# Kernel optimization log

Hardware: AMD Instinct MI355X
Metric: run time of the kernel (lower is better)

Reference implementation:

```python
import jax, jax.numpy as jnp
import numpy as np

D_MODEL = 1024
EXPAND = 2
HEADDIM = 64
D_STATE = 128
D_CONV = 4
D_INNER = EXPAND * D_MODEL          # 2048
NHEADS = D_INNER // HEADDIM         # 32
CONV_DIM = D_INNER + 2 * D_STATE    # x, B, C share the depthwise conv
EPS = 1e-5


def setup_inputs() -> dict:
    key = jax.random.key(0)
    ks = jax.random.split(key, 8)
    d_in_proj = 2 * D_INNER + 2 * D_STATE + NHEADS
    x = jax.random.normal(ks[0], (2, 2048, D_MODEL), jnp.float32)
    W_in = jax.random.normal(ks[1], (D_MODEL, d_in_proj), jnp.float32) * (D_MODEL ** -0.5)
    conv_w = jax.random.normal(ks[2], (CONV_DIM, D_CONV), jnp.float32) * 0.2
    conv_b = jnp.zeros((CONV_DIM,), jnp.float32)
    # dt init: softplus(dt_bias) in [1e-3, 1e-1]  (inverse-softplus init, as in mamba_ssm)
    dt = jnp.exp(jax.random.uniform(ks[3], (NHEADS,), jnp.float32,
                                    minval=np.log(1e-3), maxval=np.log(1e-1)))
    dt_bias = dt + jnp.log(-jnp.expm1(-dt))
    A_log = jnp.log(jax.random.uniform(ks[4], (NHEADS,), jnp.float32, minval=1.0, maxval=16.0))
    D = jnp.ones((NHEADS,), jnp.float32)
    norm_w = jnp.ones((D_INNER,), jnp.float32)
    W_out = jax.random.normal(ks[5], (D_INNER, D_MODEL), jnp.float32) * (D_INNER ** -0.5)
    return dict(x=x, W_in=W_in, conv_w=conv_w, conv_b=conv_b, dt_bias=dt_bias,
                A_log=A_log, D=D, norm_w=norm_w, W_out=W_out)


def _causal_depthwise_conv(u, w, b):
    # u: (B, L, C), w: (C, K) depthwise, causal (pad K-1 on the left)
    B, L, C = u.shape
    up = jnp.pad(u, ((0, 0), (D_CONV - 1, 0), (0, 0)))
    y = b
    for k in range(D_CONV):
        y = y + up[:, k:k + L, :] * w[:, k]
    return y


def _rms(v):
    return v * jax.lax.rsqrt(jnp.mean(v * v, axis=-1, keepdims=True) + EPS)


def reference(x, W_in, conv_w, conv_b, dt_bias, A_log, D, norm_w, W_out):
    b, l, _ = x.shape
    zxbcdt = x @ W_in                                  # (b, l, 2*d_inner + 2*d_state + nheads)
    z = zxbcdt[..., :D_INNER]
    xBC = zxbcdt[..., D_INNER:D_INNER + CONV_DIM]
    dt = jax.nn.softplus(zxbcdt[..., -NHEADS:] + dt_bias)   # (b, l, h)
    xBC = jax.nn.silu(_causal_depthwise_conv(xBC, conv_w, conv_b))
    xs = xBC[..., :D_INNER].reshape(b, l, NHEADS, HEADDIM)  # (b, l, h, p)
    Bm = xBC[..., D_INNER:D_INNER + D_STATE]                 # (b, l, n)
    Cm = xBC[..., D_INNER + D_STATE:]                        # (b, l, n)
    A = -jnp.exp(A_log)                                      # (h,)
    decay = jnp.exp(dt * A)                                  # (b, l, h)

    def step(h, inp):
        dec_t, dt_t, x_t, B_t, C_t = inp   # (b,h) (b,h) (b,h,p) (b,n) (b,n)
        h = h * dec_t[:, :, None, None] + (dt_t[:, :, None] * x_t)[..., None] * B_t[:, None, None, :]
        y_t = jnp.einsum('bhpn,bn->bhp', h, C_t)
        return h, y_t

    h0 = jnp.zeros((b, NHEADS, HEADDIM, D_STATE), x.dtype)
    xs_t = (decay.transpose(1, 0, 2), dt.transpose(1, 0, 2),
            xs.transpose(1, 0, 2, 3), Bm.transpose(1, 0, 2), Cm.transpose(1, 0, 2))
    _, ys = jax.lax.scan(step, h0, xs_t)                     # ys: (l, b, h, p)
    y = ys.transpose(1, 0, 2, 3) + D[None, None, :, None] * xs
    y = y.reshape(b, l, D_INNER)
    # gated RMSNorm (RMSNormGated in mamba_ssm), then out projection
    y = _rms(y * jax.nn.silu(z)) * norm_w
    out = y @ W_out                                          # (b, l, d_model)
    # wrapper: post RMSNorm (weight freshly initialized to ones) + residual
    return _rms(out) + x
```

## Files before the change

kernel.cpp:

```cpp
#include <hip/hip_runtime.h>
#include <hip/hip_bf16.h>

#define DMODEL 1024
#define DI     2048
#define DSTATE 128
#define NH     32
#define HD     64
#define CONVD  2304
#define LSEQ   2048
#define BATCH  2
#define DPROJ  4384
#define NPAD   4480
#define EPSV   1e-5f
#define QCH    128
#define NCH    16

#define AS1 __attribute__((address_space(1)))
#define AS3 __attribute__((address_space(3)))

typedef __attribute__((ext_vector_type(8))) short bf16x8;
typedef __attribute__((ext_vector_type(4))) float f32x4;

union U4 { ushort4 u; __hip_bfloat16 h[4]; };

__device__ __forceinline__ float bf2f(unsigned short u) {
  union { unsigned int i; float f; } c; c.i = ((unsigned)u) << 16; return c.f;
}
__device__ __forceinline__ ushort4 pack4(float x0, float x1, float x2, float x3) {
  U4 p;
  p.h[0] = __float2bfloat16(x0); p.h[1] = __float2bfloat16(x1);
  p.h[2] = __float2bfloat16(x2); p.h[3] = __float2bfloat16(x3);
  return p.u;
}

__device__ __forceinline__ bf16x8 ldsfrag(const __hip_bfloat16* base, int row, int ke) {
  int byte = row * 256 + ke * 2;
  byte ^= (row & 7) << 4;
  return *reinterpret_cast<const bf16x8*>(reinterpret_cast<const char*>(base) + byte);
}
__device__ __forceinline__ void ldswr4(__hip_bfloat16* base, int row, int col4, ushort4 v) {
  int byte = row * 256 + col4 * 2;
  byte ^= (row & 7) << 4;
  *reinterpret_cast<ushort4*>(reinterpret_cast<char*>(base) + byte) = v;
}
__device__ __forceinline__ void ldswr8(__hip_bfloat16* base, int row, int colElem,
                                       unsigned lo, unsigned hi) {
  int byte = row * 256 + colElem * 2;
  byte ^= (row & 7) << 4;
  uint2 v; v.x = lo; v.y = hi;
  *reinterpret_cast<uint2*>(reinterpret_cast<char*>(base) + byte) = v;
}
__device__ __forceinline__ bf16x8 frag32(const __hip_bfloat16* base, int row, int g) {
  int byte = row * 64 + (((g ^ (row >> 1)) & 3) << 4);
  return *reinterpret_cast<const bf16x8*>(reinterpret_cast<const char*>(base) + byte);
}

__device__ __forceinline__ void quadtr(unsigned a01, unsigned a23, int ql,
                                       unsigned& w01, unsigned& w23) {
  unsigned y01 = __shfl_xor((int)a01, 1), y23 = __shfl_xor((int)a23, 1);
  unsigned c01 = (ql & 1) ? ((y01 >> 16) | (a01 & 0xFFFF0000u))
                          : ((a01 & 0xFFFFu) | (y01 << 16));
  unsigned c23 = (ql & 1) ? ((y23 >> 16) | (a23 & 0xFFFF0000u))
                          : ((a23 & 0xFFFFu) | (y23 << 16));
  unsigned d01 = __shfl_xor((int)c01, 2), d23 = __shfl_xor((int)c23, 2);
  w01 = (ql & 2) ? d23 : c01;
  w23 = (ql & 2) ? c23 : d01;
}


__global__ void f32_to_bf16_kernel(const float* __restrict__ in,
                                   __hip_bfloat16* __restrict__ out, int n4) {
  int i = blockIdx.x * 256 + threadIdx.x;
  if (i >= n4) return;
  float4 v = reinterpret_cast<const float4*>(in)[i];
  reinterpret_cast<ushort4*>(out)[i] = pack4(v.x, v.y, v.z, v.w);
}

__global__ void transpose_f32_bf16(const float* __restrict__ in,
                                   __hip_bfloat16* __restrict__ out,
                                   int R, int C, int Cpad) {
  __shared__ float tile[32][33];
  int n0 = blockIdx.x * 32, k0 = blockIdx.y * 32;
  int tx = threadIdx.x, ty = threadIdx.y;
#pragma unroll
  for (int j = 0; j < 32; j += 8) {
    int k = k0 + ty + j, n = n0 + tx;
    tile[ty + j][tx] = (n < C) ? in[(size_t)k * C + n] : 0.f;
  }
  __syncthreads();
#pragma unroll
  for (int j = 0; j < 32; j += 8) {
    int n = n0 + ty + j, k = k0 + tx;
    if (n < Cpad) out[(size_t)n * R + k] = __float2bfloat16(tile[tx][ty + j]);
  }
}


template <int MODE>
__global__ __launch_bounds__(512, 2)
void gemm256_bt(const __hip_bfloat16* __restrict__ A,
                const __hip_bfloat16* __restrict__ Bt,
                __hip_bfloat16* __restrict__ Cout, int K) {
  __shared__ __hip_bfloat16 smA[4][256 * 32];
  __shared__ __hip_bfloat16 smB[4][256 * 32];
  int bm, bn, kbase, Kp;
  if constexpr (MODE == 0) {
    const int xcd = blockIdx.x & 7;
    const int i = blockIdx.x >> 3;
    bm = (xcd * 2 + (i & 1)) * 256;
    bn = (i >> 1) * 256;
    kbase = 0; Kp = K;
  } else {
    const int s = blockIdx.x >> 6;
    const int bb = blockIdx.x & 63;
    const int xcd = bb & 7;
    const int i = bb >> 3;
    bm = (xcd * 2 + (i & 1)) * 256;
    bn = (i >> 1) * 256;
    Kp = K >> 2; kbase = s * Kp;
  }
  const int tid = threadIdx.x;
  const int w = tid >> 6, lane = tid & 63;
  const int wm = w >> 2, wn = w & 3;
  const int fr = lane & 15, g = lane >> 4;
  const int srow = tid >> 2;
  const int sc = (((tid & 3) ^ ((srow >> 1) & 3)) << 3);

  f32x4 acc[8][4];
#pragma unroll
  for (int m = 0; m < 8; ++m)
#pragma unroll
    for (int n = 0; n < 4; ++n) acc[m][n] = (f32x4){0.f, 0.f, 0.f, 0.f};

  const __hip_bfloat16* aS = A + (size_t)(bm + srow) * K + kbase + sc;
  const __hip_bfloat16* bS = Bt + (size_t)(bn + srow) * K + kbase + sc;
  const int dbase = w * 512;

  auto STAGE = [&](int buf, int kt) {
    const int k0 = kt << 5;
#pragma unroll
    for (int j = 0; j < 2; ++j) {
      __builtin_amdgcn_global_load_lds((const AS1 void*)(aS + (size_t)(j * 128) * K + k0),
                                       (AS3 void*)(&smA[buf][j * 4096 + dbase]), 16, 0, 0);
      __builtin_amdgcn_global_load_lds((const AS1 void*)(bS + (size_t)(j * 128) * K + k0),
                                       (AS3 void*)(&smB[buf][j * 4096 + dbase]), 16, 0, 0);
    }
  };

  const int nt = Kp >> 5;
  STAGE(0, 0);
  STAGE(1, 1);
  for (int kt = 0; kt < nt; ++kt) {
    const int cur = kt & 3;
    if (kt + 2 < nt) {
      STAGE((kt + 2) & 3, kt + 2);
      asm volatile("s_waitcnt vmcnt(8)" ::: "memory");
    } else if (kt + 1 < nt) {
      asm volatile("s_waitcnt vmcnt(4)" ::: "memory");
    } else {
      asm volatile("s_waitcnt vmcnt(0)" ::: "memory");
    }
    __builtin_amdgcn_s_barrier();
    __builtin_amdgcn_s_setprio(1);
    bf16x8 af[8], bfv[4];
#pragma unroll
    for (int m = 0; m < 8; ++m)
      af[m] = frag32(&smA[cur][0], wm * 128 + m * 16 + fr, g);
#pragma unroll
    for (int n = 0; n < 4; ++n)
      bfv[n] = frag32(&smB[cur][0], wn * 64 + n * 16 + fr, g);
#pragma unroll
    for (int m = 0; m < 8; ++m)
#pragma unroll
      for (int n = 0; n < 4; ++n)
        acc[m][n] = __builtin_amdgcn_mfma_f32_16x16x32_bf16(af[m], bfv[n], acc[m][n], 0, 0, 0);
    __builtin_amdgcn_s_setprio(0);
  }

  const int rb = g * 4;
#pragma unroll
  for (int m = 0; m < 8; ++m)
#pragma unroll
    for (int n = 0; n < 4; ++n) {
      int row = bm + wm * 128 + m * 16 + rb;
      int col = bn + wn * 64 + n * 16 + fr;
      if constexpr (MODE == 0) {
        __hip_bfloat16* cp = Cout + (size_t)row * NPAD + col;
#pragma unroll
        for (int j = 0; j < 4; ++j)
          cp[(size_t)j * NPAD] = __float2bfloat16(acc[m][n][j]);
      } else {
        __hip_bfloat16* cp = Cout + (size_t)(blockIdx.x >> 6) * 4194304 +
                             (size_t)row * DMODEL + col;
#pragma unroll
        for (int j = 0; j < 4; ++j)
          cp[(size_t)j * DMODEL] = __float2bfloat16(acc[m][n][j]);
      }
    }
}


__global__ __launch_bounds__(256, 4)
void gemm_bt3(const __hip_bfloat16* __restrict__ A,
              const __hip_bfloat16* __restrict__ Bt,
              __hip_bfloat16* __restrict__ Cout, float* __restrict__ dtraw,
              int N, int K, int bnOff, int NT) {
  __shared__ __hip_bfloat16 smA[2][128 * 32];
  __shared__ __hip_bfloat16 smB[2][128 * 32];
  int bb = blockIdx.x;
  const int bm = (bb / NT) * 128;
  const int bn = bnOff + (bb % NT) * 128;
  const int t = threadIdx.x;
  const int w = t >> 6, lane = t & 63;
  const int wr = (w >> 1) * 64, wc = (w & 1) * 64;
  const int fr = lane & 15, g = lane >> 4;
  const int srow = lane >> 2;
  const int scol = ((lane & 3) ^ ((lane >> 3) & 3)) * 8;

  f32x4 acc[4][4];
#pragma unroll
  for (int m = 0; m < 4; ++m)
#pragma unroll
    for (int n = 0; n < 4; ++n) acc[m][n] = (f32x4){0.f, 0.f, 0.f, 0.f};

  const __hip_bfloat16* aSrc = A + (size_t)(bm + srow) * K + scol;
  const __hip_bfloat16* bSrc = Bt + (size_t)(bn + srow) * K + scol;

  auto STAGE = [&](int buf, int k0) {
#pragma unroll
    for (int j = 0; j < 2; ++j) {
      int ro = w * 32 + j * 16;
      __builtin_amdgcn_global_load_lds((const AS1 void*)(aSrc + (size_t)ro * K + k0),
                                       (AS3 void*)(&smA[buf][ro * 32]), 16, 0, 0);
      __builtin_amdgcn_global_load_lds((const AS1 void*)(bSrc + (size_t)ro * K + k0),
                                       (AS3 void*)(&smB[buf][ro * 32]), 16, 0, 0);
    }
  };

  STAGE(0, 0);
  __syncthreads();
  const int nt = K >> 5;
  int cur = 0;
  for (int kt = 0; kt < nt; ++kt) {
    if (kt + 1 < nt) STAGE(cur ^ 1, (kt + 1) << 5);
    bf16x8 af[4], bfv[4];
#pragma unroll
    for (int m = 0; m < 4; ++m) af[m] = frag32(&smA[cur][0], wr + m * 16 + fr, g);
#pragma unroll
    for (int n = 0; n < 4; ++n) bfv[n] = frag32(&smB[cur][0], wc + n * 16 + fr, g);
#pragma unroll
    for (int m = 0; m < 4; ++m)
#pragma unroll
      for (int n = 0; n < 4; ++n)
        acc[m][n] = __builtin_amdgcn_mfma_f32_16x16x32_bf16(af[m], bfv[n], acc[m][n], 0, 0, 0);
    __syncthreads();
    cur ^= 1;
  }

  const int r4 = g * 4;
  const int cn = lane & 15;
#pragma unroll
  for (int m = 0; m < 4; ++m)
#pragma unroll
    for (int n = 0; n < 4; ++n) {
      int row = bm + wr + m * 16 + r4;
      int col = bn + wc + n * 16 + cn;
      __hip_bfloat16* cp = Cout + (size_t)row * N + col;
#pragma unroll
      for (int j = 0; j < 4; ++j) {
        float v = acc[m][n][j];
        cp[(size_t)j * N] = __float2bfloat16(v);
        if (col >= DI + CONVD && col < DPROJ)
          dtraw[(size_t)(row + j) * NH + (col - (DI + CONVD))] = v;
      }
    }
}


__global__ __launch_bounds__(256)
void chunk_stats_kernel(const float* __restrict__ dtraw, const float* __restrict__ dt_bias,
                        const float* __restrict__ A_log,
                        float* __restrict__ csb, float* __restrict__ dtc,
                        float* __restrict__ swb, float* __restrict__ cumdecb,
                        float* __restrict__ pbuf) {
  int w = threadIdx.x >> 6, lane = threadIdx.x & 63;
  int bid = blockIdx.x * 4 + w;
  int c = bid & (NCH - 1);
  int h = (bid >> 4) & 31;
  int b = bid >> 9;
  int t0 = c * QCH;
  float a = expf(A_log[h]);
  float bias = dt_bias[h];
  const float* dtp = dtraw + ((size_t)b * LSEQ + t0) * NH + h;
  float r0 = dtp[lane * NH] + bias;
  float r1 = dtp[(64 + lane) * NH] + bias;
  float v0 = (r0 > 20.f) ? r0 : log1pf(expf(r0));
  float v1 = (r1 > 20.f) ? r1 : log1pf(expf(r1));
  float s0 = v0;
#pragma unroll
  for (int off = 1; off < 64; off <<= 1) {
    float tv = __shfl_up(s0, off);
    if (lane >= off) s0 += tv;
  }
  float T0 = __shfl(s0, 63);
  float s1 = v1;
#pragma unroll
  for (int off = 1; off < 64; off <<= 1) {
    float tv = __shfl_up(s1, off);
    if (lane >= off) s1 += tv;
  }
  float cs1 = s1 + T0;
  float Tt = __shfl(s1, 63) + T0;
  size_t base = (size_t)bid * 128;
  csb[base + lane] = s0;        csb[base + 64 + lane] = cs1;
  dtc[base + lane] = v0;        dtc[base + 64 + lane] = v1;
  swb[base + lane] = v0 * expf(-a * (Tt - s0));
  swb[base + 64 + lane] = v1 * expf(-a * (Tt - cs1));
  cumdecb[base + lane] = expf(-a * s0);
  cumdecb[base + 64 + lane] = expf(-a * cs1);
  if (lane == 0) pbuf[bid] = expf(-a * Tt);
}


__global__ __launch_bounds__(256)
void conv_silu_kernel(const __hip_bfloat16* __restrict__ zxb,
                      const float* __restrict__ cw,
                      const float* __restrict__ cb,
                      __hip_bfloat16* __restrict__ xbc) {
  int idx = blockIdx.x * 256 + threadIdx.x;
  if (idx >= BATCH * (LSEQ / 4) * (CONVD / 8)) return;
  int c8 = idx % (CONVD / 8);
  int bl4 = idx / (CONVD / 8);
  int l0 = (bl4 % (LSEQ / 4)) * 4;
  int b = bl4 / (LSEQ / 4);
  int c0 = c8 * 8;
  const __hip_bfloat16* src = zxb + (size_t)b * LSEQ * NPAD + DI + c0;

  float wv[8][4];
#pragma unroll
  for (int j = 0; j < 8; ++j)
    *reinterpret_cast<float4*>(wv[j]) = *reinterpret_cast<const float4*>(cw + (c0 + j) * 4);
  float bias[8];
  *reinterpret_cast<float4*>(bias) = *reinterpret_cast<const float4*>(cb + c0);
  *reinterpret_cast<float4*>(bias + 4) = *reinterpret_cast<const float4*>(cb + c0 + 4);

  float hist[7][8];
#pragma unroll
  for (int r = 0; r < 7; ++r) {
    int row = l0 - 3 + r;
    if (row >= 0) {
      uint4 v = *reinterpret_cast<const uint4*>(src + (size_t)row * NPAD);
      unsigned uu[4] = {v.x, v.y, v.z, v.w};
#pragma unroll
      for (int j = 0; j < 8; ++j)
        hist[r][j] = bf2f((j & 1) ? (unsigned short)(uu[j >> 1] >> 16)
                                  : (unsigned short)(uu[j >> 1] & 0xFFFF));
    } else {
#pragma unroll
      for (int j = 0; j < 8; ++j) hist[r][j] = 0.f;
    }
  }

#pragma unroll
  for (int t = 0; t < 4; ++t) {
    float acc[8];
#pragma unroll
    for (int j = 0; j < 8; ++j) {
      float a = bias[j];
      a = fmaf(wv[j][0], hist[t + 0][j], a);
      a = fmaf(wv[j][1], hist[t + 1][j], a);
      a = fmaf(wv[j][2], hist[t + 2][j], a);
      a = fmaf(wv[j][3], hist[t + 3][j], a);
      acc[j] = a / (1.f + expf(-a));
    }
    ushort4* dst = reinterpret_cast<ushort4*>(
        xbc + ((size_t)b * LSEQ + l0 + t) * CONVD + c0);
    dst[0] = pack4(acc[0], acc[1], acc[2], acc[3]);
    dst[1] = pack4(acc[4], acc[5], acc[6], acc[7]);
  }
}


__global__ __launch_bounds__(256, 2)
void ssd_mfma_local(const __hip_bfloat16* __restrict__ bxc,
                    const float* __restrict__ csb, const float* __restrict__ dtc,
                    const float* __restrict__ swb,
                    const float* __restrict__ A_log, const float* __restrict__ Dparm,
                    __hip_bfloat16* __restrict__ y, __hip_bfloat16* __restrict__ sbuf) {
  __shared__ __hip_bfloat16 T_B[128 * 128];
  __shared__ __hip_bfloat16 T_C[128 * 128];
  __shared__ __hip_bfloat16 T_X[64 * 128];

  const int bid = blockIdx.x;
  const int c = bid & (NCH - 1);
  const int h = (bid >> 4) & 31;
  const int b = bid >> 9;
  const int tid = threadIdx.x;
  const int w = tid >> 6, lane = tid & 63;
  const int q = lane >> 2, ql = lane & 3;
  const int t0 = c * QCH;
  const __hip_bfloat16* xc = bxc + (size_t)b * LSEQ * CONVD;
  const float a = expf(A_log[h]);
  const float Dh = Dparm[h];

  {
    const int rsub = lane >> 4;
    const int ch = lane & 15;
#pragma unroll
    for (int j = 0; j < 8; ++j) {
      int row = w * 32 + j * 4 + rsub;
      int sc_ = ch ^ (row & 7);
      const __hip_bfloat16* pB = xc + (size_t)(t0 + row) * CONVD + DI + sc_ * 8;
      __builtin_amdgcn_global_load_lds((const AS1 void*)pB,
                                       (AS3 void*)(T_B + (w * 32 + j * 4) * 128), 16, 0, 0);
      __builtin_amdgcn_global_load_lds((const AS1 void*)(pB + DSTATE),
                                       (AS3 void*)(T_C + (w * 32 + j * 4) * 128), 16, 0, 0);
    }
  }
#pragma unroll
  for (int r = 0; r < 8; ++r) {
    int gidx = w * 128 + q * 8 + r;
    int tb = (gidx & 31) * 4;
    int pb = (gidx >> 5) * 4;
    int t = tb + ql;
    ushort4 xv = *reinterpret_cast<const ushort4*>(xc + (size_t)(t0 + t) * CONVD + h * HD + pb);
    unsigned a01 = (unsigned)xv.x | ((unsigned)xv.y << 16);
    unsigned a23 = (unsigned)xv.z | ((unsigned)xv.w << 16);
    unsigned w01, w23;
    quadtr(a01, a23, ql, w01, w23);
    ldswr8(T_X, pb + ql, tb, w01, w23);
  }
  __syncthreads();

  const int fr = lane & 15;
  const int fk = (lane >> 4) * 8;
  const int rb = (lane >> 4) * 4;

  const int sR0 = (w >> 1) * 64, tC0 = (w & 1) * 64;
  f32x4 g[4][4];
#pragma unroll
  for (int m = 0; m < 4; ++m)
#pragma unroll
    for (int n = 0; n < 4; ++n) g[m][n] = (f32x4){0.f, 0.f, 0.f, 0.f};
  for (int kk = 0; kk < 128; kk += 32) {
    bf16x8 af[4], bfv[4];
#pragma unroll
    for (int m = 0; m < 4; ++m) af[m] = ldsfrag(T_B, sR0 + m * 16 + fr, kk + fk);
#pragma unroll
    for (int n = 0; n < 4; ++n) bfv[n] = ldsfrag(T_C, tC0 + n * 16 + fr, kk + fk);
#pragma unroll
    for (int m = 0; m < 4; ++m)
#pragma unroll
      for (int n = 0; n < 4; ++n)
        g[m][n] = __builtin_amdgcn_mfma_f32_16x16x32_bf16(af[m], bfv[n], g[m][n], 0, 0, 0);
  }
  __syncthreads();

  {
    const float* csp = csb + (size_t)bid * 128;
    const float* dtp = dtc + (size_t)bid * 128;
#pragma unroll
    for (int m = 0; m < 4; ++m) {
      int sb0 = sR0 + m * 16 + rb;
      float cs_s[4], dt_s[4];
#pragma unroll
      for (int j = 0; j < 4; ++j) { cs_s[j] = csp[sb0 + j]; dt_s[j] = dtp[sb0 + j]; }
#pragma unroll
      for (int n = 0; n < 4; ++n) {
        int tt = tC0 + n * 16 + fr;
        float cst = csp[tt];
        float vv[4];
#pragma unroll
        for (int j = 0; j < 4; ++j) {
          int s = sb0 + j;
          float e = __expf(-a * (cst - cs_s[j])) * dt_s[j];
          float pv = (s <= tt) ? g[m][n][j] * e : 0.f;
          vv[j] = pv + ((s == tt) ? Dh : 0.f);
        }
        ldswr4(T_B, tt, sb0, pack4(vv[0], vv[1], vv[2], vv[3]));
      }
    }
    const float* swp = swb + (size_t)bid * 128;
#pragma unroll
    for (int r = 0; r < 16; ++r) {
      int gidx = w * 256 + q * 16 + r;
      int tb = (gidx & 31) * 4;
      int nb = (gidx >> 5) * 4;
      int t = tb + ql;
      ushort4 bv = *reinterpret_cast<const ushort4*>(xc + (size_t)(t0 + t) * CONVD + DI + nb);
      float wt = swp[t];
      ushort4 sv = pack4(bf2f(bv.x) * wt, bf2f(bv.y) * wt, bf2f(bv.z) * wt, bf2f(bv.w) * wt);
      unsigned a01 = (unsigned)sv.x | ((unsigned)sv.y << 16);
      unsigned a23 = (unsigned)sv.z | ((unsigned)sv.w << 16);
      unsigned w01, w23;
      quadtr(a01, a23, ql, w01, w23);
      ldswr8(T_C, nb + ql, tb, w01, w23);
    }
  }
  __syncthreads();

  {
    int tR0 = w * 32;
    f32x4 yac[2][4];
#pragma unroll
    for (int m = 0; m < 2; ++m)
#pragma unroll
      for (int n = 0; n < 4; ++n) yac[m][n] = (f32x4){0.f, 0.f, 0.f, 0.f};
    for (int kk = 0; kk < 128; kk += 32) {
      bf16x8 af[2], bfv[4];
#pragma unroll
      for (int m = 0; m < 2; ++m) af[m] = ldsfrag(T_B, tR0 + m * 16 + fr, kk + fk);
#pragma unroll
      for (int n = 0; n < 4; ++n) bfv[n] = ldsfrag(T_X, n * 16 + fr, kk + fk);
#pragma unroll
      for (int m = 0; m < 2; ++m)
#pragma unroll
        for (int n = 0; n < 4; ++n)
          yac[m][n] = __builtin_amdgcn_mfma_f32_16x16x32_bf16(af[m], bfv[n], yac[m][n], 0, 0, 0);
    }
#pragma unroll
    for (int m = 0; m < 2; ++m)
#pragma unroll
      for (int n = 0; n < 4; ++n) {
        int trow = tR0 + m * 16 + rb;
        int pc = n * 16 + fr;
        __hip_bfloat16* yp = y + ((size_t)b * LSEQ + t0 + trow) * DI + h * HD + pc;
#pragma unroll
        for (int j = 0; j < 4; ++j)
          yp[(size_t)j * DI] = __float2bfloat16(yac[m][n][j]);
      }
  }

  {
    int pR0 = (w >> 1) * 32, nC0 = (w & 1) * 64;
    f32x4 sac[2][4];
#pragma unroll
    for (int m = 0; m < 2; ++m)
#pragma unroll
      for (int n = 0; n < 4; ++n) sac[m][n] = (f32x4){0.f, 0.f, 0.f, 0.f};
    for (int kk = 0; kk < 128; kk += 32) {
      bf16x8 af[2], bfv[4];
#pragma unroll
      for (int m = 0; m < 2; ++m) af[m] = ldsfrag(T_X, pR0 + m * 16 + fr, kk + fk);
#pragma unroll
      for (int n = 0; n < 4; ++n) bfv[n] = ldsfrag(T_C, nC0 + n * 16 + fr, kk + fk);
#pragma unroll
      for (int m = 0; m < 2; ++m)
#pragma unroll
        for (int n = 0; n < 4; ++n)
          sac[m][n] = __builtin_amdgcn_mfma_f32_16x16x32_bf16(af[m], bfv[n], sac[m][n], 0, 0, 0);
    }
    __hip_bfloat16* sg = sbuf + (size_t)bid * 8192;
#pragma unroll
    for (int m = 0; m < 2; ++m)
#pragma unroll
      for (int n = 0; n < 4; ++n) {
        int p = pR0 + m * 16 + rb;
        int nn = nC0 + n * 16 + fr;
#pragma unroll
        for (int j = 0; j < 4; ++j)
          sg[(size_t)(p + j) * 128 + nn] = __float2bfloat16(sac[m][n][j]);
      }
  }
}


__global__ void ssd_prop_kernel(__hip_bfloat16* __restrict__ sbuf,
                                const float* __restrict__ pbuf) {
  int idx = blockIdx.x * 256 + threadIdx.x;
  int bh = idx >> 13;
  int e = idx & 8191;
  __hip_bfloat16* base = sbuf + (size_t)bh * NCH * 8192 + e;
  const float* pb = pbuf + bh * NCH;
  float hs = 0.f;
  for (int cc = 0; cc < NCH; ++cc) {
    float sc = __bfloat162float(base[(size_t)cc * 8192]);
    base[(size_t)cc * 8192] = __float2bfloat16(hs);
    hs = fmaf(hs, pb[cc], sc);
  }
}


__global__ __launch_bounds__(256, 4)
void ssd_mfma_corr(const __hip_bfloat16* __restrict__ bxc, const __hip_bfloat16* __restrict__ sbuf,
                   const float* __restrict__ cumdecb, __hip_bfloat16* __restrict__ y) {
  const int bid = (blockIdx.x / 15) * 16 + 1 + (blockIdx.x % 15);
  const int h = (bid >> 4) & 31;
  const int b = bid >> 9;
  const int tid = threadIdx.x;
  const int w = tid >> 6, lane = tid & 63;
  const int t0 = (bid & (NCH - 1)) * QCH;
  const __hip_bfloat16* xc = bxc + (size_t)b * LSEQ * CONVD;
  const __hip_bfloat16* hsb = sbuf + (size_t)bid * 8192;
  const int fr = lane & 15;
  const int fk = (lane >> 4) * 8;
  const int rb = (lane >> 4) * 4;
  const int tR0 = w * 32;

  f32x4 ac[2][4];
#pragma unroll
  for (int m = 0; m < 2; ++m)
#pragma unroll
    for (int n = 0; n < 4; ++n) ac[m][n] = (f32x4){0.f, 0.f, 0.f, 0.f};

#pragma unroll
  for (int kk = 0; kk < 128; kk += 32) {
    bf16x8 af[2], bfv[4];
#pragma unroll
    for (int m = 0; m < 2; ++m)
      af[m] = *reinterpret_cast<const bf16x8*>(
          xc + (size_t)(t0 + tR0 + m * 16 + fr) * CONVD + DI + DSTATE + kk + fk);
#pragma unroll
    for (int n = 0; n < 4; ++n)
      bfv[n] = *reinterpret_cast<const bf16x8*>(hsb + (size_t)(n * 16 + fr) * 128 + kk + fk);
#pragma unroll
    for (int m = 0; m < 2; ++m)
#pragma unroll
      for (int n = 0; n < 4; ++n)
        ac[m][n] = __builtin_amdgcn_mfma_f32_16x16x32_bf16(af[m], bfv[n], ac[m][n], 0, 0, 0);
  }

  const float* cdp = cumdecb + (size_t)bid * 128;
#pragma unroll
  for (int m = 0; m < 2; ++m) {
    int trow = tR0 + m * 16 + rb;
    float cd[4];
#pragma unroll
    for (int j = 0; j < 4; ++j) cd[j] = cdp[trow + j];
#pragma unroll
    for (int n = 0; n < 4; ++n) {
      int pc = n * 16 + fr;
      __hip_bfloat16* yp = y + ((size_t)b * LSEQ + t0 + trow) * DI + h * HD + pc;
#pragma unroll
      for (int j = 0; j < 4; ++j) {
        float old = __bfloat162float(yp[(size_t)j * DI]);
        yp[(size_t)j * DI] = __float2bfloat16(old + cd[j] * ac[m][n][j]);
      }
    }
  }
}


__global__ __launch_bounds__(256)
void gate_rms_kernel(const __hip_bfloat16* __restrict__ y, const __hip_bfloat16* __restrict__ zxb,
                     const float* __restrict__ nw, __hip_bfloat16* __restrict__ g) {
  int row = blockIdx.x;
  int t = threadIdx.x;
  int c0 = t * 8;
  const __hip_bfloat16* yr = y + (size_t)row * DI + c0;
  const __hip_bfloat16* zr = zxb + (size_t)row * NPAD + c0;
  ushort4 y0 = *reinterpret_cast<const ushort4*>(yr);
  ushort4 y1 = *reinterpret_cast<const ushort4*>(yr + 4);
  ushort4 z0 = *reinterpret_cast<const ushort4*>(zr);
  ushort4 z1 = *reinterpret_cast<const ushort4*>(zr + 4);
  float zf[8] = {bf2f(z0.x), bf2f(z0.y), bf2f(z0.z), bf2f(z0.w),
                 bf2f(z1.x), bf2f(z1.y), bf2f(z1.z), bf2f(z1.w)};
  float yf[8] = {bf2f(y0.x), bf2f(y0.y), bf2f(y0.z), bf2f(y0.w),
                 bf2f(y1.x), bf2f(y1.y), bf2f(y1.z), bf2f(y1.w)};
  float v[8];
  float ss = 0.f;
#pragma unroll
  for (int j = 0; j < 8; ++j) {
    float z = zf[j];
    float vv = yf[j] * (z / (1.f + expf(-z)));
    v[j] = vv;
    ss += vv * vv;
  }
#pragma unroll
  for (int off = 32; off; off >>= 1) ss += __shfl_down(ss, off);
  __shared__ float red[4];
  if ((t & 63) == 0) red[t >> 6] = ss;
  __syncthreads();
  float tot = red[0] + red[1] + red[2] + red[3];
  float rstd = rsqrtf(tot * (1.f / DI) + EPSV);
  float4 na = *reinterpret_cast<const float4*>(nw + c0);
  float4 nb = *reinterpret_cast<const float4*>(nw + c0 + 4);
  ushort4 o0 = pack4(v[0] * rstd * na.x, v[1] * rstd * na.y,
                     v[2] * rstd * na.z, v[3] * rstd * na.w);
  ushort4 o1v = pack4(v[4] * rstd * nb.x, v[5] * rstd * nb.y,
                      v[6] * rstd * nb.z, v[7] * rstd * nb.w);
  ushort4* gp = reinterpret_cast<ushort4*>(g + (size_t)row * DI + c0);
  gp[0] = o0;
  gp[1] = o1v;
}


__global__ __launch_bounds__(256)
void final_rms_add(const __hip_bfloat16* __restrict__ o1p, const float* __restrict__ x,
                   float* __restrict__ out) {
  int row = blockIdx.x;
  int t = threadIdx.x;
  int c0 = t * 4;
  size_t off = (size_t)row * DMODEL + c0;
  float4 o = {0.f, 0.f, 0.f, 0.f};
#pragma unroll
  for (int s = 0; s < 4; ++s) {
    ushort4 p = *reinterpret_cast<const ushort4*>(o1p + (size_t)s * 4194304 + off);
    o.x += bf2f(p.x); o.y += bf2f(p.y); o.z += bf2f(p.z); o.w += bf2f(p.w);
  }
  float ss = o.x * o.x + o.y * o.y + o.z * o.z + o.w * o.w;
#pragma unroll
  for (int off2 = 32; off2; off2 >>= 1) ss += __shfl_down(ss, off2);
  __shared__ float red[4];
  if ((t & 63) == 0) red[t >> 6] = ss;
  __syncthreads();
  float tot = red[0] + red[1] + red[2] + red[3];
  float rstd = rsqrtf(tot * (1.f / DMODEL) + EPSV);
  float4 xv = *reinterpret_cast<const float4*>(x + off);
  float4 r;
  r.x = o.x * rstd + xv.x;
  r.y = o.y * rstd + xv.y;
  r.z = o.z * rstd + xv.z;
  r.w = o.w * rstd + xv.w;
  *reinterpret_cast<float4*>(out + off) = r;
}


extern "C" void kernel_launch(void* const* d_in, const int* in_sizes, int n_in,
                              void* d_out, int out_size, void* d_ws, size_t ws_size,
                              hipStream_t stream) {
  const float* x       = (const float*)d_in[0];
  const float* W_in    = (const float*)d_in[1];
  const float* conv_w  = (const float*)d_in[2];
  const float* conv_b  = (const float*)d_in[3];
  const float* dt_bias = (const float*)d_in[4];
  const float* A_log   = (const float*)d_in[5];
  const float* Dp      = (const float*)d_in[6];
  const float* norm_w  = (const float*)d_in[7];
  const float* W_out   = (const float*)d_in[8];
  float* out = (float*)d_out;

  float* zxF  = (float*)d_ws;
  __hip_bfloat16* zxb = (__hip_bfloat16*)zxF;
  __hip_bfloat16* o1p = zxb;
  float* xbcF = zxF + (size_t)18350080;
  __hip_bfloat16* xbc = (__hip_bfloat16*)xbcF;
  float* ybufF = xbcF + (size_t)9437184;
  __hip_bfloat16* ybuf = (__hip_bfloat16*)ybufF;
  float* dtraw = ybufF + (size_t)8388608;
  float* cumdecb = dtraw + (size_t)131072;
  __hip_bfloat16* xbf   = (__hip_bfloat16*)(cumdecb + 131072);
  __hip_bfloat16* wtin  = xbf + (size_t)4194304;
  __hip_bfloat16* wtout = wtin + (size_t)4587520;
  float* pbuf = (float*)(wtout + (size_t)2097152);
  float* csb  = pbuf + 1024;
  float* dtc  = csb + (size_t)131072;
  float* swb  = dtc + (size_t)131072;
  __hip_bfloat16* sbuf = xbf;
  __hip_bfloat16* gbf = xbf;

  f32_to_bf16_kernel<<<4096, 256, 0, stream>>>(x, xbf, 1048576);
  transpose_f32_bf16<<<dim3(140, 32), dim3(32, 8), 0, stream>>>(W_in, wtin, 1024, 4384, 4480);
  transpose_f32_bf16<<<dim3(32, 64), dim3(32, 8), 0, stream>>>(W_out, wtout, 2048, 1024, 1024);

  gemm256_bt<0><<<256, 512, 0, stream>>>(xbf, wtin, zxb, 1024);
  gemm_bt3<<<96, 256, 0, stream>>>(xbf, wtin, zxb, dtraw, NPAD, 1024, 4096, 3);

  chunk_stats_kernel<<<256, 256, 0, stream>>>(dtraw, dt_bias, A_log, csb, dtc, swb, cumdecb, pbuf);
  conv_silu_kernel<<<1152, 256, 0, stream>>>(zxb, conv_w, conv_b, xbc);

  ssd_mfma_local<<<1024, 256, 0, stream>>>(xbc, csb, dtc, swb, A_log, Dp, ybuf, sbuf);
  ssd_prop_kernel<<<2048, 256, 0, stream>>>(sbuf, pbuf);
  ssd_mfma_corr<<<960, 256, 0, stream>>>(xbc, sbuf, cumdecb, ybuf);

  gate_rms_kernel<<<4096, 256, 0, stream>>>(ybuf, zxb, norm_w, gbf);

  gemm256_bt<1><<<256, 512, 0, stream>>>(gbf, wtout, o1p, 2048);

  final_rms_add<<<4096, 256, 0, stream>>>(o1p, x, out);
}
```

Baseline: 201.8 us.

## Merge input prep kernels into one launch and retile conv to 4ch x 8 steps

Combines the x-to-bf16 cast and both weight transposes into a single prep kernel dispatched by block index, removing two kernel launches and their gaps. Separately, the causal conv kernel now handles 4 channels over 8 time steps per thread instead of 8 channels over 4 steps. This cuts redundant halo row reads per output but uses narrower 8-byte loads and stores. The prep merge adds a branch per block.

```diff
diff --git a/kernel.cpp b/kernel.cpp
--- a/kernel.cpp
+++ b/kernel.cpp
@@ -68,20 +68,31 @@
 }
 
 
-__global__ void f32_to_bf16_kernel(const float* __restrict__ in,
-                                   __hip_bfloat16* __restrict__ out, int n4) {
-  int i = blockIdx.x * 256 + threadIdx.x;
-  if (i >= n4) return;
-  float4 v = reinterpret_cast<const float4*>(in)[i];
-  reinterpret_cast<ushort4*>(out)[i] = pack4(v.x, v.y, v.z, v.w);
-}
-
-__global__ void transpose_f32_bf16(const float* __restrict__ in,
-                                   __hip_bfloat16* __restrict__ out,
-                                   int R, int C, int Cpad) {
+__global__ __launch_bounds__(256)
+void prep_kernel(const float* __restrict__ x, __hip_bfloat16* __restrict__ xbf,
+                 const float* __restrict__ W_in, __hip_bfloat16* __restrict__ wtin,
+                 const float* __restrict__ W_out, __hip_bfloat16* __restrict__ wtout) {
   __shared__ float tile[32][33];
-  int n0 = blockIdx.x * 32, k0 = blockIdx.y * 32;
-  int tx = threadIdx.x, ty = threadIdx.y;
+  const int b = blockIdx.x, tid = threadIdx.x;
+  if (b < 4096) {
+    int i = b * 256 + tid;
+    float4 v = reinterpret_cast<const float4*>(x)[i];
+    reinterpret_cast<ushort4*>(xbf)[i] = pack4(v.x, v.y, v.z, v.w);
+    return;
+  }
+  const float* in;
+  __hip_bfloat16* outp;
+  int R, C, Cpad, n0, k0;
+  if (b < 4096 + 4480) {
+    int t = b - 4096;
+    in = W_in; outp = wtin; R = 1024; C = 4384; Cpad = 4480;
+    n0 = (t % 140) * 32; k0 = (t / 140) * 32;
+  } else {
+    int t = b - 8576;
+    in = W_out; outp = wtout; R = 2048; C = 1024; Cpad = 1024;
+    n0 = (t % 32) * 32; k0 = (t / 32) * 32;
+  }
+  int tx = tid & 31, ty = tid >> 5;
 #pragma unroll
   for (int j = 0; j < 32; j += 8) {
     int k = k0 + ty + j, n = n0 + tx;
@@ -91,7 +102,7 @@
 #pragma unroll
   for (int j = 0; j < 32; j += 8) {
     int n = n0 + ty + j, k = k0 + tx;
-    if (n < Cpad) out[(size_t)n * R + k] = __float2bfloat16(tile[tx][ty + j]);
+    if (n < Cpad) outp[(size_t)n * R + k] = __float2bfloat16(tile[tx][ty + j]);
   }
 }
 
@@ -328,44 +339,40 @@
                       const float* __restrict__ cb,
                       __hip_bfloat16* __restrict__ xbc) {
   int idx = blockIdx.x * 256 + threadIdx.x;
-  if (idx >= BATCH * (LSEQ / 4) * (CONVD / 8)) return;
-  int c8 = idx % (CONVD / 8);
-  int bl4 = idx / (CONVD / 8);
-  int l0 = (bl4 % (LSEQ / 4)) * 4;
-  int b = bl4 / (LSEQ / 4);
-  int c0 = c8 * 8;
+  if (idx >= BATCH * (LSEQ / 8) * (CONVD / 4)) return;
+  int c4 = idx % (CONVD / 4);
+  int bl8 = idx / (CONVD / 4);
+  int l0 = (bl8 % (LSEQ / 8)) * 8;
+  int b = bl8 / (LSEQ / 8);
+  int c0 = c4 * 4;
   const __hip_bfloat16* src = zxb + (size_t)b * LSEQ * NPAD + DI + c0;
 
-  float wv[8][4];
-#pragma unroll
-  for (int j = 0; j < 8; ++j)
+  float wv[4][4];
+#pragma unroll
+  for (int j = 0; j < 4; ++j)
     *reinterpret_cast<float4*>(wv[j]) = *reinterpret_cast<const float4*>(cw + (c0 + j) * 4);
-  float bias[8];
+  float bias[4];
   *reinterpret_cast<float4*>(bias) = *reinterpret_cast<const float4*>(cb + c0);
-  *reinterpret_cast<float4*>(bias + 4) = *reinterpret_cast<const float4*>(cb + c0 + 4);
-
-  float hist[7][8];
-#pragma unroll
-  for (int r = 0; r < 7; ++r) {
+
+  float hist[11][4];
+#pragma unroll
+  for (int r = 0; r < 11; ++r) {
     int row = l0 - 3 + r;
     if (row >= 0) {
-      uint4 v = *reinterpret_cast<const uint4*>(src + (size_t)row * NPAD);
-      unsigned uu[4] = {v.x, v.y, v.z, v.w};
-#pragma unroll
-      for (int j = 0; j < 8; ++j)
-        hist[r][j] = bf2f((j & 1) ? (unsigned short)(uu[j >> 1] >> 16)
-                                  : (unsigned short)(uu[j >> 1] & 0xFFFF));
+      ushort4 v = *reinterpret_cast<const ushort4*>(src + (size_t)row * NPAD);
+      hist[r][0] = bf2f(v.x); hist[r][1] = bf2f(v.y);
+      hist[r][2] = bf2f(v.z); hist[r][3] = bf2f(v.w);
     } else {
 #pragma unroll
-      for (int j = 0; j < 8; ++j) hist[r][j] = 0.f;
-    }
-  }
-
-#pragma unroll
-  for (int t = 0; t < 4; ++t) {
-    float acc[8];
-#pragma unroll
-    for (int j = 0; j < 8; ++j) {
+      for (int j = 0; j < 4; ++j) hist[r][j] = 0.f;
+    }
+  }
+
+#pragma unroll
+  for (int t = 0; t < 8; ++t) {
+    float acc[4];
+#pragma unroll
+    for (int j = 0; j < 4; ++j) {
       float a = bias[j];
       a = fmaf(wv[j][0], hist[t + 0][j], a);
       a = fmaf(wv[j][1], hist[t + 1][j], a);
@@ -373,10 +380,8 @@
       a = fmaf(wv[j][3], hist[t + 3][j], a);
       acc[j] = a / (1.f + expf(-a));
     }
-    ushort4* dst = reinterpret_cast<ushort4*>(
-        xbc + ((size_t)b * LSEQ + l0 + t) * CONVD + c0);
-    dst[0] = pack4(acc[0], acc[1], acc[2], acc[3]);
-    dst[1] = pack4(acc[4], acc[5], acc[6], acc[7]);
+    *reinterpret_cast<ushort4*>(xbc + ((size_t)b * LSEQ + l0 + t) * CONVD + c0) =
+        pack4(acc[0], acc[1], acc[2], acc[3]);
   }
 }
 
@@ -749,9 +754,7 @@
   __hip_bfloat16* sbuf = xbf;
   __hip_bfloat16* gbf = xbf;
 
-  f32_to_bf16_kernel<<<4096, 256, 0, stream>>>(x, xbf, 1048576);
-  transpose_f32_bf16<<<dim3(140, 32), dim3(32, 8), 0, stream>>>(W_in, wtin, 1024, 4384, 4480);
-  transpose_f32_bf16<<<dim3(32, 64), dim3(32, 8), 0, stream>>>(W_out, wtout, 2048, 1024, 1024);
+  prep_kernel<<<10624, 256, 0, stream>>>(x, xbf, W_in, wtin, W_out, wtout);
 
   gemm256_bt<0><<<256, 512, 0, stream>>>(xbf, wtin, zxb, 1024);
   gemm_bt3<<<96, 256, 0, stream>>>(xbf, wtin, zxb, dtraw, NPAD, 1024, 4096, 3);
```

Result: faster. 194.9 us (-3.4%).
